# Performance work log

Measured on AMD Instinct MI355X. Metric: run time of the kernel, lower is better.

The kernel has to match this reference:

```python
import jax, jax.numpy as jnp
import numpy as np


def grid_sample_bilinear(feat, grid):
    """Bilinear grid_sample, align_corners=False, zeros padding.
    feat: [B, C, H, W]; grid: [B, N, 2] with (x, y) in [-1, 1]. Returns [B, C, N].
    """
    B, C, H, W = feat.shape
    gx, gy = grid[..., 0], grid[..., 1]
    # unnormalize (align_corners=False): pixel = ((g + 1) * size - 1) / 2
    ix = ((gx + 1.0) * W - 1.0) * 0.5
    iy = ((gy + 1.0) * H - 1.0) * 0.5
    x0 = jnp.floor(ix)
    y0 = jnp.floor(iy)
    x1 = x0 + 1.0
    y1 = y0 + 1.0
    wx1 = ix - x0
    wx0 = 1.0 - wx1
    wy1 = iy - y0
    wy0 = 1.0 - wy1
    featf = feat.reshape(B, C, H * W)

    def corner(xi, yi, w):
        valid = (xi >= 0) & (xi <= W - 1) & (yi >= 0) & (yi <= H - 1)
        xi_c = jnp.clip(xi, 0, W - 1).astype(jnp.int32)
        yi_c = jnp.clip(yi, 0, H - 1).astype(jnp.int32)
        idx = yi_c * W + xi_c                                  # [B, N]
        vals = jnp.take_along_axis(featf, idx[:, None, :], axis=2)  # [B, C, N]
        return vals * (w * valid.astype(feat.dtype))[:, None, :]

    return (corner(x0, y0, wx0 * wy0) + corner(x1, y0, wx1 * wy0)
            + corner(x0, y1, wx0 * wy1) + corner(x1, y1, wx1 * wy1))


def setup_inputs() -> dict:
    key = jax.random.key(0)
    ks = jax.random.split(key, 8)
    B_T, C, H, W = 128, 256, 64, 64
    J = 17
    n_heads, n_points = 8, 4
    HP = n_heads * n_points
    video_features = jax.random.normal(ks[0], (B_T, C, H, W), dtype=jnp.float32)
    reference_points = jax.random.uniform(ks[1], (B_T, J, 2), dtype=jnp.float32,
                                          minval=-1.0, maxval=1.0)
    # offset predictor: Linear(C -> HP*2); weights init small like the module
    W_off = 0.01 * jax.random.normal(ks[2], (C, HP * 2), dtype=jnp.float32)
    b_off = 0.01 * jax.random.normal(ks[3], (HP * 2,), dtype=jnp.float32)
    # weight predictor: Linear(C -> HP)
    W_w = 0.01 * jax.random.normal(ks[4], (C, HP), dtype=jnp.float32)
    b_w = jnp.zeros((HP,), dtype=jnp.float32)
    # output projection: Linear(C -> C), xavier-ish scale
    W_out = jax.random.normal(ks[5], (C, C), dtype=jnp.float32) * (1.0 / np.sqrt(C))
    b_out = jnp.zeros((C,), dtype=jnp.float32)
    return {"video_features": video_features, "reference_points": reference_points,
            "W_off": W_off, "b_off": b_off, "W_w": W_w, "b_w": b_w,
            "W_out": W_out, "b_out": b_out}


def reference(video_features, reference_points, W_off, b_off, W_w, b_w, W_out, b_out):
    B, C, H, W = video_features.shape
    J = reference_points.shape[1]
    HP = W_w.shape[1]  # n_heads * n_points
    # initial queries: sample features at reference points -> [B, J, C]
    q = grid_sample_bilinear(video_features, reference_points).transpose(0, 2, 1)
    # learned fractional offsets: [B, J, HP, 2]
    offsets = (q @ W_off + b_off).reshape(B, J, HP, 2)
    # softmax attention weights over all heads*points: [B, J, HP]
    weights = jax.nn.softmax(q @ W_w + b_w, axis=-1)
    # final sampling grid, clamped to valid range: [B, J*HP, 2]
    grid = jnp.clip(reference_points[:, :, None, :] + offsets, -1.0, 1.0)
    grid = grid.reshape(B, J * HP, 2)
    # sample and weighted-sum: [B, C, J, HP] x [B, J, HP] -> [B, J, C]
    sampled = grid_sample_bilinear(video_features, grid).reshape(B, C, J, HP)
    out = jnp.einsum('bcjp,bjp->bjc', sampled, weights)
    return out @ W_out + b_out
```

## Files before the change

### kernel.cpp

```cpp
#include <hip/hip_runtime.h>

#define B_  128
#define C_  256
#define H_  64
#define W_  64
#define J_  17
#define HP_ 32
#define HW_ (H_ * W_)
#define CG_ 4

__global__ __launch_bounds__(256)
void pass12_kernel(const float* __restrict__ feat,
                   const float* __restrict__ refpts,
                   const float* __restrict__ Woff,
                   const float* __restrict__ boff,
                   const float* __restrict__ Ww,
                   const float* __restrict__ bw,
                   int4*  __restrict__ meta_idx,
                   float4* __restrict__ meta_w)
{
    __shared__ float q_lds[C_];
    __shared__ float off_lds[2 * HP_];

    const int bj = blockIdx.x;
    const int b  = bj / J_;
    const int j  = bj % J_;
    const int c  = threadIdx.x;

    const float rx = refpts[(b * J_ + j) * 2 + 0];
    const float ry = refpts[(b * J_ + j) * 2 + 1];

    {
        const float* featbc = feat + (size_t)(b * C_ + c) * HW_;
        float ix = (rx + 1.0f) * (0.5f * W_) - 0.5f;
        float iy = (ry + 1.0f) * (0.5f * H_) - 0.5f;
        float x0f = floorf(ix), y0f = floorf(iy);
        int x0 = (int)x0f, y0 = (int)y0f;
        int x1 = x0 + 1,  y1 = y0 + 1;
        float wx1 = ix - x0f, wx0 = 1.0f - wx1;
        float wy1 = iy - y0f, wy0 = 1.0f - wy1;
        bool vx0 = (x0 >= 0) && (x0 < W_);
        bool vx1 = (x1 >= 0) && (x1 < W_);
        bool vy0 = (y0 >= 0) && (y0 < H_);
        bool vy1 = (y1 >= 0) && (y1 < H_);
        int x0c = min(max(x0, 0), W_ - 1), x1c = min(max(x1, 0), W_ - 1);
        int y0c = min(max(y0, 0), H_ - 1), y1c = min(max(y1, 0), H_ - 1);
        float v00 = (vx0 && vy0) ? featbc[y0c * W_ + x0c] : 0.0f;
        float v10 = (vx1 && vy0) ? featbc[y0c * W_ + x1c] : 0.0f;
        float v01 = (vx0 && vy1) ? featbc[y1c * W_ + x0c] : 0.0f;
        float v11 = (vx1 && vy1) ? featbc[y1c * W_ + x1c] : 0.0f;
        q_lds[c] = v00 * (wx0 * wy0) + v10 * (wx1 * wy0)
                 + v01 * (wx0 * wy1) + v11 * (wx1 * wy1);
    }
    __syncthreads();

    __shared__ float logit_lds[HP_];
    if (c < 64) {
        float s = boff[c];
        #pragma unroll 4
        for (int k = 0; k < C_; ++k) s += q_lds[k] * Woff[k * 64 + c];
        off_lds[c] = s;
    } else if (c < 96) {
        const int p = c - 64;
        float s = bw[p];
        #pragma unroll 4
        for (int k = 0; k < C_; ++k) s += q_lds[k] * Ww[k * HP_ + p];
        logit_lds[p] = s;
    }
    __syncthreads();

    if (c < HP_) {
        float l = logit_lds[c];
        float m = l;
        #pragma unroll
        for (int mask = 16; mask >= 1; mask >>= 1) m = fmaxf(m, __shfl_xor(m, mask));
        float e = expf(l - m);
        float s = e;
        #pragma unroll
        for (int mask = 16; mask >= 1; mask >>= 1) s += __shfl_xor(s, mask);
        const float ww = e / s;

        float gx = fminf(fmaxf(rx + off_lds[2 * c + 0], -1.0f), 1.0f);
        float gy = fminf(fmaxf(ry + off_lds[2 * c + 1], -1.0f), 1.0f);
        float ix = (gx + 1.0f) * (0.5f * W_) - 0.5f;
        float iy = (gy + 1.0f) * (0.5f * H_) - 0.5f;
        float x0f = floorf(ix), y0f = floorf(iy);
        int x0 = (int)x0f, y0 = (int)y0f;
        int x1 = x0 + 1,  y1 = y0 + 1;
        float wx1 = ix - x0f, wx0 = 1.0f - wx1;
        float wy1 = iy - y0f, wy0 = 1.0f - wy1;
        float v00 = (float)((x0 >= 0) && (x0 < W_) && (y0 >= 0) && (y0 < H_));
        float v10 = (float)((x1 >= 0) && (x1 < W_) && (y0 >= 0) && (y0 < H_));
        float v01 = (float)((x0 >= 0) && (x0 < W_) && (y1 >= 0) && (y1 < H_));
        float v11 = (float)((x1 >= 0) && (x1 < W_) && (y1 >= 0) && (y1 < H_));
        int x0c = min(max(x0, 0), W_ - 1), x1c = min(max(x1, 0), W_ - 1);
        int y0c = min(max(y0, 0), H_ - 1), y1c = min(max(y1, 0), H_ - 1);
        const int mi = bj * HP_ + c;
        meta_idx[mi] = make_int4(y0c * W_ + x0c, y0c * W_ + x1c,
                                 y1c * W_ + x0c, y1c * W_ + x1c);
        meta_w[mi] = make_float4(ww * wx0 * wy0 * v00, ww * wx1 * wy0 * v10,
                                 ww * wx0 * wy1 * v01, ww * wx1 * wy1 * v11);
    }
}

__global__ __launch_bounds__(256)
void gather_kernel(const float* __restrict__ feat,
                   const int4*  __restrict__ meta_idx,
                   const float4* __restrict__ meta_w,
                   float* __restrict__ acc)
{
    __shared__ float plane[CG_ * HW_];

    const int blk = blockIdx.x;
    const int b   = blk >> 6;
    const int cg  = blk & 63;
    const int c0  = cg * CG_;
    const int t   = threadIdx.x;

    #pragma unroll
    for (int k = 0; k < CG_; ++k) {
        const float4* src = (const float4*)(feat + (size_t)(b * C_ + c0 + k) * HW_);
        float4* dst = (float4*)(plane + k * HW_);
        #pragma unroll
        for (int i = 0; i < 4; ++i)
            dst[t + i * 256] = src[t + i * 256];
    }
    __syncthreads();

    const int wv   = t >> 6;
    const int ln   = t & 63;
    const int p    = ln & 31;
    const int half = ln >> 5;

    #pragma unroll
    for (int iter = 0; iter < 3; ++iter) {
        const int j = iter * 8 + wv * 2 + half;
        float pj0 = 0.0f, pj1 = 0.0f, pj2 = 0.0f, pj3 = 0.0f;
        if (j < J_) {
            const int mi = (b * J_ + j) * HP_ + p;
            const int4   id = meta_idx[mi];
            const float4 w  = meta_w[mi];
            pj0 = w.x * plane[0 * HW_ + id.x] + w.y * plane[0 * HW_ + id.y]
                + w.z * plane[0 * HW_ + id.z] + w.w * plane[0 * HW_ + id.w];
            pj1 = w.x * plane[1 * HW_ + id.x] + w.y * plane[1 * HW_ + id.y]
                + w.z * plane[1 * HW_ + id.z] + w.w * plane[1 * HW_ + id.w];
            pj2 = w.x * plane[2 * HW_ + id.x] + w.y * plane[2 * HW_ + id.y]
                + w.z * plane[2 * HW_ + id.z] + w.w * plane[2 * HW_ + id.w];
            pj3 = w.x * plane[3 * HW_ + id.x] + w.y * plane[3 * HW_ + id.y]
                + w.z * plane[3 * HW_ + id.z] + w.w * plane[3 * HW_ + id.w];
        }
        #pragma unroll
        for (int mask = 16; mask >= 1; mask >>= 1) {
            pj0 += __shfl_xor(pj0, mask);
            pj1 += __shfl_xor(pj1, mask);
            pj2 += __shfl_xor(pj2, mask);
            pj3 += __shfl_xor(pj3, mask);
        }
        if (j < J_ && p == 0) {
            float4* dst = (float4*)(acc + ((size_t)(b * J_ + j)) * C_ + c0);
            *dst = make_float4(pj0, pj1, pj2, pj3);
        }
    }
}

__global__ __launch_bounds__(256)
void proj_kernel(const float* __restrict__ acc,
                 const float* __restrict__ Wout,
                 const float* __restrict__ bout,
                 float* __restrict__ out)
{
    __shared__ float a_lds[C_];
    const int bj = blockIdx.x;
    const int c  = threadIdx.x;
    a_lds[c] = acc[(size_t)bj * C_ + c];
    __syncthreads();
    float o = bout[c];
    #pragma unroll 4
    for (int k = 0; k < C_; ++k) o += a_lds[k] * Wout[k * C_ + c];
    out[(size_t)bj * C_ + c] = o;
}

__device__ __forceinline__ float bilin_sample(const float* __restrict__ featc,
                                              float gx, float gy) {
    float ix = (gx + 1.0f) * (0.5f * W_) - 0.5f;
    float iy = (gy + 1.0f) * (0.5f * H_) - 0.5f;
    float x0f = floorf(ix), y0f = floorf(iy);
    int x0 = (int)x0f, y0 = (int)y0f;
    int x1 = x0 + 1,  y1 = y0 + 1;
    float wx1 = ix - x0f, wx0 = 1.0f - wx1;
    float wy1 = iy - y0f, wy0 = 1.0f - wy1;
    bool vx0 = (x0 >= 0) && (x0 < W_);
    bool vx1 = (x1 >= 0) && (x1 < W_);
    bool vy0 = (y0 >= 0) && (y0 < H_);
    bool vy1 = (y1 >= 0) && (y1 < H_);
    int x0c = min(max(x0, 0), W_ - 1), x1c = min(max(x1, 0), W_ - 1);
    int y0c = min(max(y0, 0), H_ - 1), y1c = min(max(y1, 0), H_ - 1);
    float v00 = (vx0 && vy0) ? featc[y0c * W_ + x0c] : 0.0f;
    float v10 = (vx1 && vy0) ? featc[y0c * W_ + x1c] : 0.0f;
    float v01 = (vx0 && vy1) ? featc[y1c * W_ + x0c] : 0.0f;
    float v11 = (vx1 && vy1) ? featc[y1c * W_ + x1c] : 0.0f;
    return v00 * (wx0 * wy0) + v10 * (wx1 * wy0)
         + v01 * (wx0 * wy1) + v11 * (wx1 * wy1);
}

__global__ __launch_bounds__(256)
void msdks_kernel(const float* __restrict__ feat,
                  const float* __restrict__ refpts,
                  const float* __restrict__ Woff,
                  const float* __restrict__ boff,
                  const float* __restrict__ Ww,
                  const float* __restrict__ bw,
                  const float* __restrict__ Wout,
                  const float* __restrict__ bout,
                  float* __restrict__ out)
{
    __shared__ float q_lds[C_];
    __shared__ float off_lds[2 * HP_];
    __shared__ float logit_lds[HP_];
    __shared__ float wgt_lds[HP_];
    __shared__ float gx_lds[HP_];
    __shared__ float gy_lds[HP_];
    __shared__ float acc_lds[C_];

    const int bj = blockIdx.x;
    const int b  = bj / J_;
    const int j  = bj % J_;
    const int c  = threadIdx.x;

    const float rx = refpts[(b * J_ + j) * 2 + 0];
    const float ry = refpts[(b * J_ + j) * 2 + 1];
    const float* featbc = feat + (size_t)(b * C_ + c) * HW_;

    q_lds[c] = bilin_sample(featbc, rx, ry);
    __syncthreads();

    if (c < 64) {
        float s = boff[c];
        for (int k = 0; k < C_; ++k) s += q_lds[k] * Woff[k * 64 + c];
        off_lds[c] = s;
    } else if (c < 96) {
        const int p = c - 64;
        float s = bw[p];
        for (int k = 0; k < C_; ++k) s += q_lds[k] * Ww[k * HP_ + p];
        logit_lds[p] = s;
    }
    __syncthreads();

    if (c < HP_) {
        float l = logit_lds[c];
        float m = l;
        for (int mask = 16; mask; mask >>= 1) m = fmaxf(m, __shfl_xor(m, mask));
        float e = expf(l - m);
        float s = e;
        for (int mask = 16; mask; mask >>= 1) s += __shfl_xor(s, mask);
        wgt_lds[c] = e / s;
        gx_lds[c] = fminf(fmaxf(rx + off_lds[c * 2 + 0], -1.0f), 1.0f);
        gy_lds[c] = fminf(fmaxf(ry + off_lds[c * 2 + 1], -1.0f), 1.0f);
    }
    __syncthreads();

    float acc = 0.0f;
    for (int pp = 0; pp < HP_; ++pp)
        acc += wgt_lds[pp] * bilin_sample(featbc, gx_lds[pp], gy_lds[pp]);
    acc_lds[c] = acc;
    __syncthreads();

    float o = bout[c];
    for (int k = 0; k < C_; ++k) o += acc_lds[k] * Wout[k * C_ + c];
    out[(size_t)(b * J_ + j) * C_ + c] = o;
}

extern "C" void kernel_launch(void* const* d_in, const int* in_sizes, int n_in,
                              void* d_out, int out_size, void* d_ws, size_t ws_size,
                              hipStream_t stream) {
    const float* feat   = (const float*)d_in[0];
    const float* refpts = (const float*)d_in[1];
    const float* Woff   = (const float*)d_in[2];
    const float* boff   = (const float*)d_in[3];
    const float* Ww     = (const float*)d_in[4];
    const float* bw     = (const float*)d_in[5];
    const float* Wout   = (const float*)d_in[6];
    const float* bout   = (const float*)d_in[7];
    float* out = (float*)d_out;

    const size_t n_meta    = (size_t)B_ * J_ * HP_;
    const size_t idx_bytes = n_meta * sizeof(int4);
    const size_t w_bytes   = n_meta * sizeof(float4);
    const size_t acc_bytes = (size_t)B_ * J_ * C_ * sizeof(float);

    if (ws_size >= idx_bytes + w_bytes + acc_bytes) {
        char* ws = (char*)d_ws;
        int4*   meta_idx = (int4*)ws;
        float4* meta_w   = (float4*)(ws + idx_bytes);
        float*  acc      = (float*)(ws + idx_bytes + w_bytes);

        pass12_kernel<<<dim3(B_ * J_), dim3(256), 0, stream>>>(
            feat, refpts, Woff, boff, Ww, bw, meta_idx, meta_w);
        gather_kernel<<<dim3(B_ * (C_ / CG_)), dim3(256), 0, stream>>>(
            feat, meta_idx, meta_w, acc);
        proj_kernel<<<dim3(B_ * J_), dim3(256), 0, stream>>>(
            acc, Wout, bout, out);
    } else {
        msdks_kernel<<<dim3(B_ * J_), dim3(256), 0, stream>>>(
            feat, refpts, Woff, boff, Ww, bw, Wout, bout, out);
    }
}
```

Baseline: 191.6 us.

## Split-K the small matvecs across all waves and halve gather channel group

The offset/weight and output projection matvecs are reworked so that all four waves each handle a quarter of the K dimension, with the partial sums reduced through LDS, where before only one or two waves did the serial 256-long loop. The gather kernel now stages 2 channels per block instead of 4. That halves LDS use per block (32KB), which allows more resident blocks and doubles the grid to improve occupancy. The cost is extra LDS reductions and syncs, plus redundant metadata loads because each metadata entry is now read by twice as many blocks.

Measured after the change: 177.5 us. -7.4%, faster.

```diff
diff --git a/kernel.cpp b/kernel.cpp
--- a/kernel.cpp
+++ b/kernel.cpp
@@ -7,7 +7,7 @@
 #define J_  17
 #define HP_ 32
 #define HW_ (H_ * W_)
-#define CG_ 4
+#define CG_ 2
 
 __global__ __launch_bounds__(256)
 void pass12_kernel(const float* __restrict__ feat,
@@ -20,7 +20,10 @@
                    float4* __restrict__ meta_w)
 {
     __shared__ float q_lds[C_];
+    __shared__ float part_off[4][64];
+    __shared__ float part_w[4][32];
     __shared__ float off_lds[2 * HP_];
+    __shared__ float logit_lds[HP_];
 
     const int bj = blockIdx.x;
     const int b  = bj / J_;
@@ -54,18 +57,27 @@
     }
     __syncthreads();
 
-    __shared__ float logit_lds[HP_];
+    {
+        const int wv = c >> 6, ln = c & 63;
+        float aoff = 0.0f, aw = 0.0f;
+        #pragma unroll 8
+        for (int i = 0; i < 64; ++i) {
+            const int k = wv * 64 + i;
+            const float qv = q_lds[k];
+            aoff += qv * Woff[k * 64 + ln];
+            if (ln < 32) aw += qv * Ww[k * 32 + ln];
+        }
+        part_off[wv][ln] = aoff;
+        if (ln < 32) part_w[wv][ln] = aw;
+    }
+    __syncthreads();
     if (c < 64) {
-        float s = boff[c];
-        #pragma unroll 4
-        for (int k = 0; k < C_; ++k) s += q_lds[k] * Woff[k * 64 + c];
-        off_lds[c] = s;
+        off_lds[c] = boff[c] + part_off[0][c] + part_off[1][c]
+                   + part_off[2][c] + part_off[3][c];
     } else if (c < 96) {
         const int p = c - 64;
-        float s = bw[p];
-        #pragma unroll 4
-        for (int k = 0; k < C_; ++k) s += q_lds[k] * Ww[k * HP_ + p];
-        logit_lds[p] = s;
+        logit_lds[p] = bw[p] + part_w[0][p] + part_w[1][p]
+                     + part_w[2][p] + part_w[3][p];
     }
     __syncthreads();
 
@@ -112,17 +124,16 @@
     __shared__ float plane[CG_ * HW_];
 
     const int blk = blockIdx.x;
-    const int b   = blk >> 6;
-    const int cg  = blk & 63;
+    const int b   = blk >> 7;
+    const int cg  = blk & 127;
     const int c0  = cg * CG_;
     const int t   = threadIdx.x;
 
-    #pragma unroll
-    for (int k = 0; k < CG_; ++k) {
-        const float4* src = (const float4*)(feat + (size_t)(b * C_ + c0 + k) * HW_);
-        float4* dst = (float4*)(plane + k * HW_);
+    {
+        const float4* src = (const float4*)(feat + (size_t)(b * C_ + c0) * HW_);
+        float4* dst = (float4*)plane;
         #pragma unroll
-        for (int i = 0; i < 4; ++i)
+        for (int i = 0; i < 8; ++i)
             dst[t + i * 256] = src[t + i * 256];
     }
     __syncthreads();
@@ -135,30 +146,24 @@
     #pragma unroll
     for (int iter = 0; iter < 3; ++iter) {
         const int j = iter * 8 + wv * 2 + half;
-        float pj0 = 0.0f, pj1 = 0.0f, pj2 = 0.0f, pj3 = 0.0f;
+        float pj0 = 0.0f, pj1 = 0.0f;
         if (j < J_) {
             const int mi = (b * J_ + j) * HP_ + p;
             const int4   id = meta_idx[mi];
             const float4 w  = meta_w[mi];
-            pj0 = w.x * plane[0 * HW_ + id.x] + w.y * plane[0 * HW_ + id.y]
-                + w.z * plane[0 * HW_ + id.z] + w.w * plane[0 * HW_ + id.w];
-            pj1 = w.x * plane[1 * HW_ + id.x] + w.y * plane[1 * HW_ + id.y]
-                + w.z * plane[1 * HW_ + id.z] + w.w * plane[1 * HW_ + id.w];
-            pj2 = w.x * plane[2 * HW_ + id.x] + w.y * plane[2 * HW_ + id.y]
-                + w.z * plane[2 * HW_ + id.z] + w.w * plane[2 * HW_ + id.w];
-            pj3 = w.x * plane[3 * HW_ + id.x] + w.y * plane[3 * HW_ + id.y]
-                + w.z * plane[3 * HW_ + id.z] + w.w * plane[3 * HW_ + id.w];
+            pj0 = w.x * plane[id.x] + w.y * plane[id.y]
+                + w.z * plane[id.z] + w.w * plane[id.w];
+            pj1 = w.x * plane[HW_ + id.x] + w.y * plane[HW_ + id.y]
+                + w.z * plane[HW_ + id.z] + w.w * plane[HW_ + id.w];
         }
         #pragma unroll
         for (int mask = 16; mask >= 1; mask >>= 1) {
             pj0 += __shfl_xor(pj0, mask);
             pj1 += __shfl_xor(pj1, mask);
-            pj2 += __shfl_xor(pj2, mask);
-            pj3 += __shfl_xor(pj3, mask);
         }
         if (j < J_ && p == 0) {
-            float4* dst = (float4*)(acc + ((size_t)(b * J_ + j)) * C_ + c0);
-            *dst = make_float4(pj0, pj1, pj2, pj3);
+            float2* dst = (float2*)(acc + ((size_t)(b * J_ + j)) * C_ + c0);
+            *dst = make_float2(pj0, pj1);
         }
     }
 }
@@ -170,14 +175,32 @@
                  float* __restrict__ out)
 {
     __shared__ float a_lds[C_];
+    __shared__ float partial[4][C_];
     const int bj = blockIdx.x;
-    const int c  = threadIdx.x;
-    a_lds[c] = acc[(size_t)bj * C_ + c];
-    __syncthreads();
-    float o = bout[c];
-    #pragma unroll 4
-    for (int k = 0; k < C_; ++k) o += a_lds[k] * Wout[k * C_ + c];
-    out[(size_t)bj * C_ + c] = o;
+    const int t  = threadIdx.x;
+    a_lds[t] = acc[(size_t)bj * C_ + t];
+    __syncthreads();
+
+    const int wv = t >> 6, ln = t & 63;
+    float s0 = 0.0f, s1 = 0.0f, s2 = 0.0f, s3 = 0.0f;
+    #pragma unroll 8
+    for (int i = 0; i < 64; ++i) {
+        const int k = wv * 64 + i;
+        const float qv = a_lds[k];
+        const float* row = Wout + (size_t)k * C_;
+        s0 += qv * row[ln];
+        s1 += qv * row[ln + 64];
+        s2 += qv * row[ln + 128];
+        s3 += qv * row[ln + 192];
+    }
+    partial[wv][ln]       = s0;
+    partial[wv][ln + 64]  = s1;
+    partial[wv][ln + 128] = s2;
+    partial[wv][ln + 192] = s3;
+    __syncthreads();
+
+    float o = bout[t] + partial[0][t] + partial[1][t] + partial[2][t] + partial[3][t];
+    out[(size_t)bj * C_ + t] = o;
 }
 
 __device__ __forceinline__ float bilin_sample(const float* __restrict__ featc,
```
